# Optimization experiments

Measured on AMD Instinct MI355X. Metric: run time of the kernel, lower is better.

## Reference

```python
import jax, jax.numpy as jnp
import numpy as np

B, C, H = 4, 64, 48
HEADS, BSWIN = 2, 4
BIG = [3, 6, 12, 24]      # big window edge per scale (cubic)
SMALL = [1, 2, 4, 8]      # small (pool) window edge per scale
NH = 3                    # small windows per big window per dim (= big/small)
L = NH ** 3               # tokens per big window after pooling
CPH = C // (HEADS * BSWIN)  # channels per head per scale = 8


def _rel_pos_index():
    coords = np.stack(np.meshgrid(*([np.arange(NH)] * 3), indexing='ij')).reshape(3, -1)
    rel = coords[:, :, None] - coords[:, None, :] + (NH - 1)
    span = 2 * NH - 1
    return jnp.asarray(rel[0] * span * span + rel[1] * span + rel[2])  # (L, L) int

REL_IDX = _rel_pos_index()


def _interp_matrix(n_in, n_out):
    # 1D linear interpolation matrix, align_corners=True (matches F.interpolate)
    if n_out == n_in:
        return jnp.eye(n_in, dtype=jnp.float32)
    pos = jnp.arange(n_out, dtype=jnp.float32) * (n_in - 1) / (n_out - 1)
    i0 = jnp.clip(jnp.floor(pos).astype(jnp.int32), 0, n_in - 2)
    w = pos - i0.astype(jnp.float32)
    r = jnp.arange(n_out)
    m = jnp.zeros((n_out, n_in), jnp.float32)
    return m.at[r, i0].add(1.0 - w).at[r, i0 + 1].add(w)


def _gather(x):
    # x: (B, C, H, H, H) -> (B, HEADS, sum_N, L, CPH)
    b = x.shape[0]
    x = x.reshape(b, BSWIN, HEADS, CPH, H, H, H)
    parts, Ns = [], []
    for i in range(BSWIN):
        bw, sw = BIG[i], SMALL[i]
        N1 = H // bw
        xi = x[:, i].reshape(b, HEADS, CPH, N1, NH, sw, N1, NH, sw, N1, NH, sw)
        xi = xi.max(axis=(5, 8, 11))  # max-pool each small window
        # (b, head, c, Nh, nh, Nw, nw, Nd, nd) -> b head (Nh Nw Nd) (nh nw nd) c
        xi = xi.transpose(0, 1, 3, 5, 7, 4, 6, 8, 2)
        parts.append(xi.reshape(b, HEADS, N1 ** 3, L, CPH))
        Ns.append(N1)
    return jnp.concatenate(parts, axis=2), Ns


def _scatter(attn, Ns):
    # attn: (B, HEADS, sum_N, L, CPH) -> (B, C, H, H, H)
    b = attn.shape[0]
    outs, idx = [], 0
    for i in range(BSWIN):
        bw, sw = BIG[i], SMALL[i]
        N1 = Ns[i]
        N = N1 ** 3
        o = attn[:, :, idx:idx + N].reshape(b, HEADS, N, NH, NH, NH, CPH)
        M = _interp_matrix(NH, bw)  # trilinear upsample by small window size
        o = jnp.einsum('bhnijkc,pi,qj,rk->bhnpqrc', o, M, M, M)
        o = o.reshape(b, HEADS, N1, N1, N1, bw, bw, bw, CPH)
        # b head Nh Nw Nd wh ww wd c -> b head c (Nh wh) (Nw ww) (Nd wd)
        o = o.transpose(0, 1, 8, 2, 5, 3, 6, 4, 7).reshape(b, HEADS, CPH, H, H, H)
        outs.append(o)
        idx += N
    out = jnp.stack(outs, axis=1)  # b bswin head c h w d
    return out.reshape(b, C, H, H, H)


def _attention(q, k, v, rpb_table):
    c = q.shape[-1]
    scores = jnp.einsum('bhNmc,bhNnc->bhNmn', q, k) / jnp.sqrt(jnp.asarray(c, q.dtype))
    w = jax.nn.softmax(scores, axis=-1)
    bias = rpb_table[REL_IDX].transpose(2, 0, 1)  # (head, L, L), added POST-softmax
    w = w + bias[None, :, None]
    return jnp.einsum('bhNmn,bhNnc->bhNmc', w, v)


def setup_inputs() -> dict:
    key = jax.random.key(0)
    kq, kk, kv, kp = jax.random.split(key, 4)
    shp = (B, C, H, H, H)
    return {
        'query': jax.random.normal(kq, shp, jnp.float32),
        'key': jax.random.normal(kk, shp, jnp.float32),
        'value': jax.random.normal(kv, shp, jnp.float32),
        'rpb_table': jax.random.normal(kp, ((2 * NH - 1) ** 3, HEADS), jnp.float32) * 0.02,
    }


def reference(query, key, value, rpb_table):
    q, Ns = _gather(query)
    k, _ = _gather(key)
    v, _ = _gather(value)
    attn = _attention(q, k, v, rpb_table)
    return _scatter(attn, Ns)
```

## Files before the change

### kernel.cpp

```cpp
#include <hip/hip_runtime.h>


typedef unsigned short u16;
static constexpr long S1 = 4L * 48 * 24 * 24 * 24;

typedef float f4 __attribute__((ext_vector_type(4)));
typedef u16 us8 __attribute__((ext_vector_type(8)));
typedef u16 us4 __attribute__((ext_vector_type(4)));

__device__ __forceinline__ f4 ntload(const float* p) {
    return __builtin_nontemporal_load((const f4*)p);
}
__device__ __forceinline__ void ntstore(float* p, f4 v) {
    __builtin_nontemporal_store(v, (f4*)p);
}
__device__ __forceinline__ f4 vmax4(f4 a, f4 b) {
    f4 r;
    r[0] = fmaxf(a[0], b[0]); r[1] = fmaxf(a[1], b[1]);
    r[2] = fmaxf(a[2], b[2]); r[3] = fmaxf(a[3], b[3]);
    return r;
}
__device__ __forceinline__ float b2f(u16 u) {
    union { unsigned int i; float f; } c; c.i = ((unsigned int)u) << 16; return c.f;
}
__device__ __forceinline__ u16 f2b(float x) {
    union { float f; unsigned int i; } c; c.f = x;
    unsigned int b = c.i;
    return (u16)((b + 0x7FFFu + ((b >> 16) & 1u)) >> 16);
}

__device__ __forceinline__ void pool1_body(int pid,
                                           const float* __restrict__ q,
                                           const float* __restrict__ k,
                                           const float* __restrict__ v,
                                           u16* __restrict__ P1)
{
    const int tz = pid % 3;
    int rest = pid / 3;
    const int zc = rest % 12; rest /= 12;
    const int c = rest % 48;
    const int b = rest / 48;
    const float* in = tz == 0 ? q : (tz == 1 ? k : v);
    u16* o = P1 + (long)tz * S1;
    const float* base = in + ((long)b * 64 + 16 + c) * 110592;

    for (int i = threadIdx.x; i < 288; i += 256) {
        const int zl = i / 144;
        const int rem = i % 144;
        const int oy = rem / 6;
        const int qx = rem % 6;
        const int oz = zc * 2 + zl;
        const float* p = base + ((long)(2 * oz) * 48 + 2 * oy) * 48 + qx * 8;
        f4 r0a = ntload(p),        r0b = ntload(p + 4);
        f4 r1a = ntload(p + 48),   r1b = ntload(p + 52);
        f4 r2a = ntload(p + 2304), r2b = ntload(p + 2308);
        f4 r3a = ntload(p + 2352), r3b = ntload(p + 2356);
        f4 ma = vmax4(vmax4(r0a, r1a), vmax4(r2a, r3a));
        f4 mb = vmax4(vmax4(r0b, r1b), vmax4(r2b, r3b));
        us4 res;
        res[0] = f2b(fmaxf(ma[0], ma[1]));
        res[1] = f2b(fmaxf(ma[2], ma[3]));
        res[2] = f2b(fmaxf(mb[0], mb[1]));
        res[3] = f2b(fmaxf(mb[2], mb[3]));
        long oaddr = (((long)b * 48 + c) * 24 + oz) * 576 + oy * 24 + qx * 4;
        *(us4*)(o + oaddr) = res;
    }
}

__device__ __forceinline__ void attn0_body(int aid, float* smem,
                                           const float* __restrict__ qsrc,
                                           const float* __restrict__ ksrc,
                                           const float* __restrict__ vsrc,
                                           const float* __restrict__ rpb,
                                           float* __restrict__ out)
{
    float* tile = smem;
    float* bias = smem + 5376;
    const int tid = threadIdx.x;
    int rest = aid;
    const int half = rest & 1; rest >>= 1;
    const int Wy = rest % 16; rest /= 16;
    const int Wz = rest % 16; rest /= 16;
    const int head = rest % 2;
    const int b = rest / 2;

    for (int i = tid; i < 729; i += 256) {
        int m = i / 27, n = i % 27;
        int mi = m / 9, mj = (m / 3) % 3, mk = m % 3;
        int ni = n / 9, nj = (n / 3) % 3, nk = n % 3;
        int ridx = (mi - ni + 2) * 25 + (mj - nj + 2) * 5 + (mk - nk + 2);
        bias[i] = rpb[ridx * 2 + head];
    }

    for (int i = tid; i < 1296; i += 256) {
        int seg = i / 6;
        int off = (i % 6) * 4;
        int tz = seg / 72;
        int rem = seg % 72;
        int cph = rem / 9;
        int rem2 = rem % 9;
        int zt = rem2 / 3;
        int r = rem2 % 3;
        const float* src = tz == 0 ? qsrc : (tz == 1 ? ksrc : vsrc);
        long addr = ((((long)b * 64 + head * 8 + cph) * 48 + 3 * Wz + zt) * 48
                     + 3 * Wy + r) * 48 + half * 24 + off;
        f4 f = ntload(src + addr);
#pragma unroll
        for (int j = 0; j < 4; j++) {
            int xl = off + j;
            int wxl = xl / 3, tk = xl - wxl * 3;
            int tok = zt * 9 + r * 3 + tk;
            tile[((wxl * 3 + tz) * 8 + cph) * 28 + tok] = f[j];
        }
    }
    __syncthreads();

    const int wx = tid >> 5;
    const int lane = tid & 31;
    if (lane < 27) {
        const int m = lane;
        float* b0 = tile + wx * 672;
        const float* kb = b0 + 224;
        const float* vb = b0 + 448;
        float qr[8];
#pragma unroll
        for (int c = 0; c < 8; c++) qr[c] = b0[c * 28 + m];
        float s[27];
        float mx = -1e30f;
#pragma unroll
        for (int n = 0; n < 27; n++) {
            float acc = 0.f;
#pragma unroll
            for (int c = 0; c < 8; c++) acc += qr[c] * kb[c * 28 + n];
            acc *= 0.35355339059327373f;
            s[n] = acc;
            mx = fmaxf(mx, acc);
        }
        float sum = 0.f;
#pragma unroll
        for (int n = 0; n < 27; n++) {
            s[n] = __expf(s[n] - mx);
            sum += s[n];
        }
        float rs = 1.0f / sum;
        float o[8] = {0, 0, 0, 0, 0, 0, 0, 0};
#pragma unroll
        for (int n = 0; n < 27; n++) {
            float w = s[n] * rs + bias[m * 27 + n];
#pragma unroll
            for (int c = 0; c < 8; c++) o[c] += w * vb[c * 28 + n];
        }
#pragma unroll
        for (int c = 0; c < 8; c++) b0[c * 28 + m] = o[c];
    }
    __syncthreads();

    for (int i = tid; i < 432; i += 256) {
        int x4i = i % 6;
        int t2 = i / 6;
        int cph = t2 % 8; t2 /= 8;
        int y = t2 % 3;
        int zl = t2 / 3;
        f4 res;
#pragma unroll
        for (int e = 0; e < 4; e++) {
            int xl = x4i * 4 + e;
            int wxl = xl / 3, tk = xl - wxl * 3;
            int tok = zl * 9 + y * 3 + tk;
            res[e] = tile[wxl * 672 + cph * 28 + tok];
        }
        int z = 3 * Wz + zl;
        int Y = 3 * Wy + y;
        long oaddr = (((long)(b * 64 + head * 8 + cph) * 48 + z) * 48 + Y) * 48
                     + half * 24 + x4i * 4;
        ntstore(out + oaddr, res);
    }
}

__global__ void fused_k1(const float* __restrict__ q, const float* __restrict__ k,
                         const float* __restrict__ v, const float* __restrict__ rpb,
                         u16* __restrict__ P1, float* __restrict__ out)
{
    __shared__ __align__(16) float smem[6105];
    const int bx = blockIdx.x;
    if (bx < 8192 && (bx & 1) == 0) {
        attn0_body(bx >> 1, smem, q, k, v, rpb, out);
    } else {
        int pid = (bx < 8192) ? (bx >> 1) : (bx - 4096);
        pool1_body(pid, q, k, v, P1);
    }
}

static constexpr int WS = 676;

__device__ __forceinline__ void load_bias(float* bias, const float* __restrict__ rpb,
                                          int head, int tid)
{
    for (int i = tid; i < 729; i += 256) {
        int m = i / 27, n = i % 27;
        int mi = m / 9, mj = (m / 3) % 3, mk = m % 3;
        int ni = n / 9, nj = (n / 3) % 3, nk = n % 3;
        int ridx = (mi - ni + 2) * 25 + (mj - nj + 2) * 5 + (mk - nk + 2);
        bias[i] = rpb[ridx * 2 + head];
    }
}

__device__ __forceinline__ void attn_tile(float* tile, const float* bias, int tid, int NW)
{
    const int wx = tid >> 5;
    const int lane = tid & 31;
    if (wx < NW && lane < 27) {
        const int m = lane;
        float* b0 = tile + wx * WS;
        const float* kb = b0 + 224;
        const float* vb = b0 + 448;
        float qr[8];
#pragma unroll
        for (int c = 0; c < 8; c++) qr[c] = b0[c * 28 + m];
        float s[27];
        float mx = -1e30f;
#pragma unroll
        for (int n = 0; n < 27; n++) {
            float acc = 0.f;
#pragma unroll
            for (int c = 0; c < 8; c++) acc += qr[c] * kb[c * 28 + n];
            acc *= 0.35355339059327373f;
            s[n] = acc;
            mx = fmaxf(mx, acc);
        }
        float sum = 0.f;
#pragma unroll
        for (int n = 0; n < 27; n++) {
            s[n] = __expf(s[n] - mx);
            sum += s[n];
        }
        float rs = 1.0f / sum;
        float o[8] = {0, 0, 0, 0, 0, 0, 0, 0};
#pragma unroll
        for (int n = 0; n < 27; n++) {
            float w = s[n] * rs + bias[m * 27 + n];
#pragma unroll
            for (int c = 0; c < 8; c++) o[c] += w * vb[c * 28 + n];
        }
#pragma unroll
        for (int c = 0; c < 8; c++) b0[c * 28 + m] = o[c];
    }
}

__device__ __forceinline__ void preblend(const float* bp, int i0p, int i0q,
                                         float w00, float w01, float w10, float w11,
                                         float* v)
{
#pragma unroll
    for (int kx = 0; kx < 3; kx++) {
        const float* t = bp + i0p * 9 + i0q * 3 + kx;
        v[kx] = w00 * t[0] + w01 * t[3] + w10 * t[9] + w11 * t[12];
    }
}

__global__ void fused_k2(const u16* __restrict__ P1, const float* __restrict__ rpb,
                         float* __restrict__ out)
{
    __shared__ __align__(16) float smem[8 * WS + 729];
    float* tile = smem;
    float* bias = smem + 8 * WS;
    const int tid = threadIdx.x;
    const int bx = blockIdx.x;

    if (bx >= 1024) {
        int aid = bx - 1024;
        const int Wy = aid % 8; aid /= 8;
        const int Wz = aid % 8; aid /= 8;
        const int head = aid % 2;
        const int b = aid / 2;
        load_bias(bias, rpb, head, tid);
        for (int i = tid; i < 648; i += 256) {
            int xq = i % 3;
            int row = i / 3;
            int tz = row / 72;
            int rem = row % 72;
            int cph = rem / 9;
            int rem2 = rem % 9;
            int zt = rem2 / 3, r = rem2 % 3;
            const u16* p = P1 + (long)tz * S1 + ((long)b * 48 + head * 8 + cph) * 13824
                           + (3 * Wz + zt) * 576 + (3 * Wy + r) * 24 + xq * 8;
            us8 u = *(const us8*)p;
#pragma unroll
            for (int j = 0; j < 8; j++) {
                int xl = xq * 8 + j;
                int wxl = xl / 3, tk = xl - wxl * 3;
                tile[wxl * WS + (tz * 8 + cph) * 28 + zt * 9 + r * 3 + tk] = b2f(u[j]);
            }
        }
        __syncthreads();
        attn_tile(tile, bias, tid, 8);
        __syncthreads();

        const float inv = 2.0f / 5.0f;
        for (int i = tid; i < 3456; i += 256) {
            int x4 = i % 12;
            int t2 = i / 12;
            int cph = t2 % 8; t2 /= 8;
            int wq = t2 % 6;
            int wp = t2 / 6;
            float posp = wp * inv; int i0p = min((int)posp, 1); float fp = posp - (float)i0p;
            float posq = wq * inv; int i0q = min((int)posq, 1); float fq = posq - (float)i0q;
            float w00 = (1.f - fp) * (1.f - fq), w01 = (1.f - fp) * fq;
            float w10 = fp * (1.f - fq),         w11 = fp * fq;
            int Wa = (4 * x4) / 6, Wb = (4 * x4 + 3) / 6;
            float va[3], vb2[3];
            preblend(tile + Wa * WS + cph * 28, i0p, i0q, w00, w01, w10, w11, va);
            preblend(tile + Wb * WS + cph * 28, i0p, i0q, w00, w01, w10, w11, vb2);
            f4 res;
#pragma unroll
            for (int e = 0; e < 4; e++) {
                int xg = 4 * x4 + e;
                int Wx = xg / 6, wr = xg - 6 * Wx;
                const float* vv = (Wx == Wa) ? va : vb2;
                float posr = wr * inv; int i0r = min((int)posr, 1); float fr = posr - (float)i0r;
                res[e] = (1.f - fr) * vv[i0r] + fr * vv[i0r + 1];
            }
            long oaddr = (((long)(b * 64 + 16 + head * 8 + cph) * 48 + 6 * Wz + wp) * 48
                          + 6 * Wy + wq) * 48 + x4 * 4;
            ntstore(out + oaddr, res);
        }
    } else if (bx >= 512) {
        int bid = bx - 512;
        const int chunk = bid % 4; bid /= 4;
        const int Wy = bid % 4; bid /= 4;
        const int Wz = bid % 4; bid /= 4;
        const int head = bid % 2;
        const int b = bid / 2;
        load_bias(bias, rpb, head, tid);
        for (int i = tid; i < 648; i += 256) {
            int xq = i % 3;
            int t = i / 3;
            int yt = t % 3; t /= 3;
            int zt = t % 3; t /= 3;
            int cph = t % 8;
            int tz = t / 8;
            const u16* base = P1 + (long)tz * S1 + ((long)b * 48 + 16 + head * 8 + cph) * 13824;
            float tv[4] = {-1e30f, -1e30f, -1e30f, -1e30f};
#pragma unroll
            for (int dz = 0; dz < 2; dz++)
#pragma unroll
                for (int dy = 0; dy < 2; dy++) {
                    const u16* p = base + (6 * Wz + 2 * zt + dz) * 576
                                   + (6 * Wy + 2 * yt + dy) * 24 + xq * 8;
                    us8 u = *(const us8*)p;
#pragma unroll
                    for (int j = 0; j < 4; j++)
                        tv[j] = fmaxf(tv[j], fmaxf(b2f(u[2 * j]), b2f(u[2 * j + 1])));
                }
#pragma unroll
            for (int j = 0; j < 4; j++) {
                int xt = xq * 4 + j;
                int wxl = xt / 3, tk = xt - wxl * 3;
                tile[wxl * WS + (tz * 8 + cph) * 28 + zt * 9 + yt * 3 + tk] = tv[j];
            }
        }
        __syncthreads();
        attn_tile(tile, bias, tid, 4);
        __syncthreads();

        const float inv = 2.0f / 11.0f;
        for (int i = tid; i < 3456; i += 256) {
            int x4 = i % 12;
            int t2 = i / 12;
            int cph = t2 % 8; t2 /= 8;
            int wq = t2 % 12;
            int wp = chunk * 3 + t2 / 12;
            float posp = wp * inv; int i0p = min((int)posp, 1); float fp = posp - (float)i0p;
            float posq = wq * inv; int i0q = min((int)posq, 1); float fq = posq - (float)i0q;
            float w00 = (1.f - fp) * (1.f - fq), w01 = (1.f - fp) * fq;
            float w10 = fp * (1.f - fq),         w11 = fp * fq;
            int W = x4 / 3;
            float v[3];
            preblend(tile + W * WS + cph * 28, i0p, i0q, w00, w01, w10, w11, v);
            f4 res;
#pragma unroll
            for (int e = 0; e < 4; e++) {
                int xg = 4 * x4 + e;
                int wr = xg - 12 * W;
                float posr = wr * inv; int i0r = min((int)posr, 1); float fr = posr - (float)i0r;
                res[e] = (1.f - fr) * v[i0r] + fr * v[i0r + 1];
            }
            long oaddr = (((long)(b * 64 + 32 + head * 8 + cph) * 48 + 12 * Wz + wp) * 48
                          + 12 * Wy + wq) * 48 + x4 * 4;
            ntstore(out + oaddr, res);
        }
    } else {
        int cid = bx;
        const int slice = cid % 8; cid /= 8;
        const int Wx = cid % 2; cid /= 2;
        const int Wy = cid % 2; cid /= 2;
        const int Wz = cid % 2; cid /= 2;
        const int head = cid % 2;
        const int b = cid / 2;
        load_bias(bias, rpb, head, tid);
        for (int i = tid; i < 216; i += 256) {
            int yt = i % 3;
            int t = i / 3;
            int zt = t % 3; t /= 3;
            int cph = t % 8;
            int tz = t / 8;
            const u16* base = P1 + (long)tz * S1 + ((long)b * 48 + 32 + head * 8 + cph) * 13824;
            float tv[3] = {-1e30f, -1e30f, -1e30f};
#pragma unroll
            for (int dz = 0; dz < 4; dz++)
#pragma unroll
                for (int dy = 0; dy < 4; dy++) {
                    const u16* p = base + (12 * Wz + 4 * zt + dz) * 576
                                   + (12 * Wy + 4 * yt + dy) * 24 + 12 * Wx;
#pragma unroll
                    for (int s3 = 0; s3 < 3; s3++) {
                        us4 u = *(const us4*)(p + 4 * s3);
                        tv[s3] = fmaxf(tv[s3],
                                       fmaxf(fmaxf(b2f(u[0]), b2f(u[1])),
                                             fmaxf(b2f(u[2]), b2f(u[3]))));
                    }
                }
#pragma unroll
            for (int s3 = 0; s3 < 3; s3++)
                tile[(tz * 8 + cph) * 28 + zt * 9 + yt * 3 + s3] = tv[s3];
        }
        __syncthreads();
        attn_tile(tile, bias, tid, 1);
        __syncthreads();

        const float inv = 2.0f / 23.0f;
        for (int i = tid; i < 3456; i += 256) {
            int x4 = i % 6;
            int t2 = i / 6;
            int cph = t2 % 8; t2 /= 8;
            int wq = t2 % 24;
            int wp = slice * 3 + t2 / 24;
            float posp = wp * inv; int i0p = min((int)posp, 1); float fp = posp - (float)i0p;
            float posq = wq * inv; int i0q = min((int)posq, 1); float fq = posq - (float)i0q;
            float w00 = (1.f - fp) * (1.f - fq), w01 = (1.f - fp) * fq;
            float w10 = fp * (1.f - fq),         w11 = fp * fq;
            float v[3];
            preblend(tile + cph * 28, i0p, i0q, w00, w01, w10, w11, v);
            f4 res;
#pragma unroll
            for (int e = 0; e < 4; e++) {
                int wr = 4 * x4 + e;
                float posr = wr * inv; int i0r = min((int)posr, 1); float fr = posr - (float)i0r;
                res[e] = (1.f - fr) * v[i0r] + fr * v[i0r + 1];
            }
            long oaddr = (((long)(b * 64 + 48 + head * 8 + cph) * 48 + 24 * Wz + wp) * 48
                          + 24 * Wy + wq) * 48 + 24 * Wx + x4 * 4;
            ntstore(out + oaddr, res);
        }
    }
}

extern "C" void kernel_launch(void* const* d_in, const int* in_sizes, int n_in,
                              void* d_out, int out_size, void* d_ws, size_t ws_size,
                              hipStream_t stream)
{
    const float* q   = (const float*)d_in[0];
    const float* k   = (const float*)d_in[1];
    const float* v   = (const float*)d_in[2];
    const float* rpb = (const float*)d_in[3];
    float* out = (float*)d_out;
    u16* P1 = (u16*)d_ws;

    fused_k1<<<11008, 256, 0, stream>>>(q, k, v, rpb, P1, out);

    fused_k2<<<1536, 256, 0, stream>>>(P1, rpb, out);
}
```

Baseline: 161.6 us.

## Fuse both kernels into one launch, pooling directly from fp32 inputs

Replaces the two-kernel scheme with a single kernel. The old scheme pooled scales 1-3 into a bf16 workspace and then re-read it. Each scale's block now max-pools its own window straight from the fp32 q/k/v inputs, which removes the workspace round trip, the bf16 rounding and one launch. In exchange, the large-scale blocks become much heavier: 64 blocks each do a 24^3 window pool plus the full upsample, and 128 blocks do 4 windows each. This creates load imbalance and long tail blocks, though those heavy blocks are placed at the start of the grid.

Result: slower. 190.5 us (+17.9%).

```diff
diff --git a/kernel.cpp b/kernel.cpp
--- a/kernel.cpp
+++ b/kernel.cpp
@@ -1,12 +1,7 @@
 #include <hip/hip_runtime.h>
 
 
-typedef unsigned short u16;
-static constexpr long S1 = 4L * 48 * 24 * 24 * 24;
-
 typedef float f4 __attribute__((ext_vector_type(4)));
-typedef u16 us8 __attribute__((ext_vector_type(8)));
-typedef u16 us4 __attribute__((ext_vector_type(4)));
 
 __device__ __forceinline__ f4 ntload(const float* p) {
     return __builtin_nontemporal_load((const f4*)p);
@@ -20,50 +15,74 @@
     r[2] = fmaxf(a[2], b[2]); r[3] = fmaxf(a[3], b[3]);
     return r;
 }
-__device__ __forceinline__ float b2f(u16 u) {
-    union { unsigned int i; float f; } c; c.i = ((unsigned int)u) << 16; return c.f;
-}
-__device__ __forceinline__ u16 f2b(float x) {
-    union { float f; unsigned int i; } c; c.f = x;
-    unsigned int b = c.i;
-    return (u16)((b + 0x7FFFu + ((b >> 16) & 1u)) >> 16);
-}
-
-__device__ __forceinline__ void pool1_body(int pid,
-                                           const float* __restrict__ q,
-                                           const float* __restrict__ k,
-                                           const float* __restrict__ v,
-                                           u16* __restrict__ P1)
-{
-    const int tz = pid % 3;
-    int rest = pid / 3;
-    const int zc = rest % 12; rest /= 12;
-    const int c = rest % 48;
-    const int b = rest / 48;
-    const float* in = tz == 0 ? q : (tz == 1 ? k : v);
-    u16* o = P1 + (long)tz * S1;
-    const float* base = in + ((long)b * 64 + 16 + c) * 110592;
-
-    for (int i = threadIdx.x; i < 288; i += 256) {
-        const int zl = i / 144;
-        const int rem = i % 144;
-        const int oy = rem / 6;
-        const int qx = rem % 6;
-        const int oz = zc * 2 + zl;
-        const float* p = base + ((long)(2 * oz) * 48 + 2 * oy) * 48 + qx * 8;
-        f4 r0a = ntload(p),        r0b = ntload(p + 4);
-        f4 r1a = ntload(p + 48),   r1b = ntload(p + 52);
-        f4 r2a = ntload(p + 2304), r2b = ntload(p + 2308);
-        f4 r3a = ntload(p + 2352), r3b = ntload(p + 2356);
-        f4 ma = vmax4(vmax4(r0a, r1a), vmax4(r2a, r3a));
-        f4 mb = vmax4(vmax4(r0b, r1b), vmax4(r2b, r3b));
-        us4 res;
-        res[0] = f2b(fmaxf(ma[0], ma[1]));
-        res[1] = f2b(fmaxf(ma[2], ma[3]));
-        res[2] = f2b(fmaxf(mb[0], mb[1]));
-        res[3] = f2b(fmaxf(mb[2], mb[3]));
-        long oaddr = (((long)b * 48 + c) * 24 + oz) * 576 + oy * 24 + qx * 4;
-        *(us4*)(o + oaddr) = res;
+__device__ __forceinline__ float hmax4(f4 v) {
+    return fmaxf(fmaxf(v[0], v[1]), fmaxf(v[2], v[3]));
+}
+
+static constexpr int WS = 676;
+
+__device__ __forceinline__ void load_bias(float* bias, const float* __restrict__ rpb,
+                                          int head, int tid)
+{
+    for (int i = tid; i < 729; i += 256) {
+        int m = i / 27, n = i % 27;
+        int mi = m / 9, mj = (m / 3) % 3, mk = m % 3;
+        int ni = n / 9, nj = (n / 3) % 3, nk = n % 3;
+        int ridx = (mi - ni + 2) * 25 + (mj - nj + 2) * 5 + (mk - nk + 2);
+        bias[i] = rpb[ridx * 2 + head];
+    }
+}
+
+__device__ __forceinline__ void attn_tile(float* tile, const float* bias, int tid, int NW)
+{
+    const int wx = tid >> 5;
+    const int lane = tid & 31;
+    if (wx < NW && lane < 27) {
+        const int m = lane;
+        float* b0 = tile + wx * WS;
+        const float* kb = b0 + 224;
+        const float* vb = b0 + 448;
+        float qr[8];
+#pragma unroll
+        for (int c = 0; c < 8; c++) qr[c] = b0[c * 28 + m];
+        float s[27];
+        float mx = -1e30f;
+#pragma unroll
+        for (int n = 0; n < 27; n++) {
+            float acc = 0.f;
+#pragma unroll
+            for (int c = 0; c < 8; c++) acc += qr[c] * kb[c * 28 + n];
+            acc *= 0.35355339059327373f;
+            s[n] = acc;
+            mx = fmaxf(mx, acc);
+        }
+        float sum = 0.f;
+#pragma unroll
+        for (int n = 0; n < 27; n++) {
+            s[n] = __expf(s[n] - mx);
+            sum += s[n];
+        }
+        float rs = 1.0f / sum;
+        float o[8] = {0, 0, 0, 0, 0, 0, 0, 0};
+#pragma unroll
+        for (int n = 0; n < 27; n++) {
+            float w = s[n] * rs + bias[m * 27 + n];
+#pragma unroll
+            for (int c = 0; c < 8; c++) o[c] += w * vb[c * 28 + n];
+        }
+#pragma unroll
+        for (int c = 0; c < 8; c++) b0[c * 28 + m] = o[c];
+    }
+}
+
+__device__ __forceinline__ void preblend(const float* bp, int i0p, int i0q,
+                                         float w00, float w01, float w10, float w11,
+                                         float* v)
+{
+#pragma unroll
+    for (int kx = 0; kx < 3; kx++) {
+        const float* t = bp + i0p * 9 + i0q * 3 + kx;
+        v[kx] = w00 * t[0] + w01 * t[3] + w10 * t[9] + w11 * t[12];
     }
 }
 
@@ -177,119 +196,180 @@
     }
 }
 
-__global__ void fused_k1(const float* __restrict__ q, const float* __restrict__ k,
-                         const float* __restrict__ v, const float* __restrict__ rpb,
-                         u16* __restrict__ P1, float* __restrict__ out)
-{
-    __shared__ __align__(16) float smem[6105];
-    const int bx = blockIdx.x;
-    if (bx < 8192 && (bx & 1) == 0) {
-        attn0_body(bx >> 1, smem, q, k, v, rpb, out);
-    } else {
-        int pid = (bx < 8192) ? (bx >> 1) : (bx - 4096);
-        pool1_body(pid, q, k, v, P1);
-    }
-}
-
-static constexpr int WS = 676;
-
-__device__ __forceinline__ void load_bias(float* bias, const float* __restrict__ rpb,
-                                          int head, int tid)
-{
-    for (int i = tid; i < 729; i += 256) {
-        int m = i / 27, n = i % 27;
-        int mi = m / 9, mj = (m / 3) % 3, mk = m % 3;
-        int ni = n / 9, nj = (n / 3) % 3, nk = n % 3;
-        int ridx = (mi - ni + 2) * 25 + (mj - nj + 2) * 5 + (mk - nk + 2);
-        bias[i] = rpb[ridx * 2 + head];
-    }
-}
-
-__device__ __forceinline__ void attn_tile(float* tile, const float* bias, int tid, int NW)
-{
-    const int wx = tid >> 5;
-    const int lane = tid & 31;
-    if (wx < NW && lane < 27) {
-        const int m = lane;
-        float* b0 = tile + wx * WS;
-        const float* kb = b0 + 224;
-        const float* vb = b0 + 448;
-        float qr[8];
-#pragma unroll
-        for (int c = 0; c < 8; c++) qr[c] = b0[c * 28 + m];
-        float s[27];
-        float mx = -1e30f;
-#pragma unroll
-        for (int n = 0; n < 27; n++) {
-            float acc = 0.f;
-#pragma unroll
-            for (int c = 0; c < 8; c++) acc += qr[c] * kb[c * 28 + n];
-            acc *= 0.35355339059327373f;
-            s[n] = acc;
-            mx = fmaxf(mx, acc);
-        }
-        float sum = 0.f;
-#pragma unroll
-        for (int n = 0; n < 27; n++) {
-            s[n] = __expf(s[n] - mx);
-            sum += s[n];
-        }
-        float rs = 1.0f / sum;
-        float o[8] = {0, 0, 0, 0, 0, 0, 0, 0};
-#pragma unroll
-        for (int n = 0; n < 27; n++) {
-            float w = s[n] * rs + bias[m * 27 + n];
-#pragma unroll
-            for (int c = 0; c < 8; c++) o[c] += w * vb[c * 28 + n];
-        }
-#pragma unroll
-        for (int c = 0; c < 8; c++) b0[c * 28 + m] = o[c];
-    }
-}
-
-__device__ __forceinline__ void preblend(const float* bp, int i0p, int i0q,
-                                         float w00, float w01, float w10, float w11,
-                                         float* v)
-{
-#pragma unroll
-    for (int kx = 0; kx < 3; kx++) {
-        const float* t = bp + i0p * 9 + i0q * 3 + kx;
-        v[kx] = w00 * t[0] + w01 * t[3] + w10 * t[9] + w11 * t[12];
-    }
-}
-
-__global__ void fused_k2(const u16* __restrict__ P1, const float* __restrict__ rpb,
-                         float* __restrict__ out)
-{
-    __shared__ __align__(16) float smem[8 * WS + 729];
+__global__ void fused_all(const float* __restrict__ q, const float* __restrict__ k,
+                          const float* __restrict__ v, const float* __restrict__ rpb,
+                          float* __restrict__ out)
+{
+    __shared__ __align__(16) float smem[6137];
     float* tile = smem;
     float* bias = smem + 8 * WS;
     const int tid = threadIdx.x;
     const int bx = blockIdx.x;
 
-    if (bx >= 1024) {
-        int aid = bx - 1024;
+    if (bx >= 704) {
+        attn0_body(bx - 704, smem, q, k, v, rpb, out);
+        return;
+    }
+
+    if (bx < 64) {
+        int cid = bx;
+        const int Wx = cid % 2; cid /= 2;
+        const int Wy = cid % 2; cid /= 2;
+        const int Wz = cid % 2; cid /= 2;
+        const int head = cid % 2;
+        const int b = cid / 2;
+        load_bias(bias, rpb, head, tid);
+
+        for (int i = tid; i < 648; i += 256) {
+            int tok = i % 27;
+            int t = i / 27;
+            int cph = t % 8;
+            int tz = t / 8;
+            const int zt = tok / 9, yt = (tok / 3) % 3, xt = tok % 3;
+            const float* in = tz == 0 ? q : (tz == 1 ? k : v);
+            const float* base = in + (((long)b * 64 + 48 + head * 8 + cph) * 48
+                                      + Wz * 24 + zt * 8) * 2304
+                                + (long)(Wy * 24 + yt * 8) * 48 + Wx * 24 + xt * 8;
+            f4 acc = ntload(base);
+            acc = vmax4(acc, ntload(base + 4));
+            for (int dz = 0; dz < 8; dz++) {
+#pragma unroll
+                for (int dy = 0; dy < 8; dy++) {
+                    if (dz == 0 && dy == 0) continue;
+                    const float* p = base + dz * 2304 + dy * 48;
+                    acc = vmax4(acc, ntload(p));
+                    acc = vmax4(acc, ntload(p + 4));
+                }
+            }
+            tile[(tz * 8 + cph) * 28 + tok] = hmax4(acc);
+        }
+        __syncthreads();
+        attn_tile(tile, bias, tid, 1);
+        __syncthreads();
+
+        const float inv = 2.0f / 23.0f;
+        for (int i = tid; i < 27648; i += 256) {
+            int x4 = i % 6;
+            int t2 = i / 6;
+            int cph = t2 % 8; t2 /= 8;
+            int wq = t2 % 24;
+            int wp = t2 / 24;
+            float posp = wp * inv; int i0p = min((int)posp, 1); float fp = posp - (float)i0p;
+            float posq = wq * inv; int i0q = min((int)posq, 1); float fq = posq - (float)i0q;
+            float w00 = (1.f - fp) * (1.f - fq), w01 = (1.f - fp) * fq;
+            float w10 = fp * (1.f - fq),         w11 = fp * fq;
+            float vv[3];
+            preblend(tile + cph * 28, i0p, i0q, w00, w01, w10, w11, vv);
+            f4 res;
+#pragma unroll
+            for (int e = 0; e < 4; e++) {
+                int wr = 4 * x4 + e;
+                float posr = wr * inv; int i0r = min((int)posr, 1); float fr = posr - (float)i0r;
+                res[e] = (1.f - fr) * vv[i0r] + fr * vv[i0r + 1];
+            }
+            long oaddr = (((long)(b * 64 + 48 + head * 8 + cph) * 48 + 24 * Wz + wp) * 48
+                          + 24 * Wy + wq) * 48 + 24 * Wx + x4 * 4;
+            ntstore(out + oaddr, res);
+        }
+    } else if (bx < 192) {
+        int bid = bx - 64;
+        const int Wy = bid % 4; bid /= 4;
+        const int Wz = bid % 4; bid /= 4;
+        const int head = bid % 2;
+        const int b = bid / 2;
+        load_bias(bias, rpb, head, tid);
+
+        for (int i = tid; i < 1296; i += 256) {
+            int xp = i % 6;
+            int t = i / 6;
+            int yt = t % 3; t /= 3;
+            int zt = t % 3; t /= 3;
+            int cph = t % 8;
+            int tz = t / 8;
+            const float* in = tz == 0 ? q : (tz == 1 ? k : v);
+            const float* base = in + (((long)b * 64 + 32 + head * 8 + cph) * 48
+                                      + Wz * 12 + zt * 4) * 2304
+                                + (long)(Wy * 12 + yt * 4) * 48 + xp * 8;
+            f4 a0 = ntload(base), a1 = ntload(base + 4);
+#pragma unroll
+            for (int dz = 0; dz < 4; dz++) {
+#pragma unroll
+                for (int dy = 0; dy < 4; dy++) {
+                    if (dz == 0 && dy == 0) continue;
+                    const float* p = base + dz * 2304 + dy * 48;
+                    a0 = vmax4(a0, ntload(p));
+                    a1 = vmax4(a1, ntload(p + 4));
+                }
+            }
+            float tv[2] = {hmax4(a0), hmax4(a1)};
+#pragma unroll
+            for (int j = 0; j < 2; j++) {
+                int xl = xp * 2 + j;
+                int wxl = xl / 3, tk = xl - wxl * 3;
+                tile[wxl * WS + (tz * 8 + cph) * 28 + zt * 9 + yt * 3 + tk] = tv[j];
+            }
+        }
+        __syncthreads();
+        attn_tile(tile, bias, tid, 4);
+        __syncthreads();
+
+        const float inv = 2.0f / 11.0f;
+        for (int i = tid; i < 13824; i += 256) {
+            int x4 = i % 12;
+            int t2 = i / 12;
+            int cph = t2 % 8; t2 /= 8;
+            int wq = t2 % 12;
+            int wp = t2 / 12;
+            float posp = wp * inv; int i0p = min((int)posp, 1); float fp = posp - (float)i0p;
+            float posq = wq * inv; int i0q = min((int)posq, 1); float fq = posq - (float)i0q;
+            float w00 = (1.f - fp) * (1.f - fq), w01 = (1.f - fp) * fq;
+            float w10 = fp * (1.f - fq),         w11 = fp * fq;
+            int W = x4 / 3;
+            float vv[3];
+            preblend(tile + W * WS + cph * 28, i0p, i0q, w00, w01, w10, w11, vv);
+            f4 res;
+#pragma unroll
+            for (int e = 0; e < 4; e++) {
+                int wr = 4 * x4 + e - 12 * W;
+                float posr = wr * inv; int i0r = min((int)posr, 1); float fr = posr - (float)i0r;
+                res[e] = (1.f - fr) * vv[i0r] + fr * vv[i0r + 1];
+            }
+            long oaddr = (((long)(b * 64 + 32 + head * 8 + cph) * 48 + 12 * Wz + wp) * 48
+                          + 12 * Wy + wq) * 48 + x4 * 4;
+            ntstore(out + oaddr, res);
+        }
+    } else {
+        int aid = bx - 192;
         const int Wy = aid % 8; aid /= 8;
         const int Wz = aid % 8; aid /= 8;
         const int head = aid % 2;
         const int b = aid / 2;
         load_bias(bias, rpb, head, tid);
-        for (int i = tid; i < 648; i += 256) {
-            int xq = i % 3;
-            int row = i / 3;
-            int tz = row / 72;
-            int rem = row % 72;
-            int cph = rem / 9;
-            int rem2 = rem % 9;
-            int zt = rem2 / 3, r = rem2 % 3;
-            const u16* p = P1 + (long)tz * S1 + ((long)b * 48 + head * 8 + cph) * 13824
-                           + (3 * Wz + zt) * 576 + (3 * Wy + r) * 24 + xq * 8;
-            us8 u = *(const us8*)p;
-#pragma unroll
-            for (int j = 0; j < 8; j++) {
-                int xl = xq * 8 + j;
+
+        for (int i = tid; i < 1296; i += 256) {
+            int qx = i % 6;
+            int t = i / 6;
+            int yt = t % 3; t /= 3;
+            int zt = t % 3; t /= 3;
+            int cph = t % 8;
+            int tz = t / 8;
+            const float* in = tz == 0 ? q : (tz == 1 ? k : v);
+            const float* base = in + (((long)b * 64 + 16 + head * 8 + cph) * 48
+                                      + Wz * 6 + zt * 2) * 2304
+                                + (long)(Wy * 6 + yt * 2) * 48 + qx * 8;
+            f4 r0a = ntload(base),        r0b = ntload(base + 4);
+            f4 r1a = ntload(base + 48),   r1b = ntload(base + 52);
+            f4 r2a = ntload(base + 2304), r2b = ntload(base + 2308);
+            f4 r3a = ntload(base + 2352), r3b = ntload(base + 2356);
+            f4 ma = vmax4(vmax4(r0a, r1a), vmax4(r2a, r3a));
+            f4 mb = vmax4(vmax4(r0b, r1b), vmax4(r2b, r3b));
+            float tv[4] = { fmaxf(ma[0], ma[1]), fmaxf(ma[2], ma[3]),
+                            fmaxf(mb[0], mb[1]), fmaxf(mb[2], mb[3]) };
+#pragma unroll
+            for (int j = 0; j < 4; j++) {
+                int xl = qx * 4 + j;
                 int wxl = xl / 3, tk = xl - wxl * 3;
-                tile[wxl * WS + (tz * 8 + cph) * 28 + zt * 9 + r * 3 + tk] = b2f(u[j]);
+                tile[wxl * WS + (tz * 8 + cph) * 28 + zt * 9 + yt * 3 + tk] = tv[j];
             }
         }
         __syncthreads();
@@ -324,134 +404,6 @@
                           + 6 * Wy + wq) * 48 + x4 * 4;
             ntstore(out + oaddr, res);
         }
-    } else if (bx >= 512) {
-        int bid = bx - 512;
-        const int chunk = bid % 4; bid /= 4;
-        const int Wy = bid % 4; bid /= 4;
-        const int Wz = bid % 4; bid /= 4;
-        const int head = bid % 2;
-        const int b = bid / 2;
-        load_bias(bias, rpb, head, tid);
-        for (int i = tid; i < 648; i += 256) {
-            int xq = i % 3;
-            int t = i / 3;
-            int yt = t % 3; t /= 3;
-            int zt = t % 3; t /= 3;
-            int cph = t % 8;
-            int tz = t / 8;
-            const u16* base = P1 + (long)tz * S1 + ((long)b * 48 + 16 + head * 8 + cph) * 13824;
-            float tv[4] = {-1e30f, -1e30f, -1e30f, -1e30f};
-#pragma unroll
-            for (int dz = 0; dz < 2; dz++)
-#pragma unroll
-                for (int dy = 0; dy < 2; dy++) {
-                    const u16* p = base + (6 * Wz + 2 * zt + dz) * 576
-                                   + (6 * Wy + 2 * yt + dy) * 24 + xq * 8;
-                    us8 u = *(const us8*)p;
-#pragma unroll
-                    for (int j = 0; j < 4; j++)
-                        tv[j] = fmaxf(tv[j], fmaxf(b2f(u[2 * j]), b2f(u[2 * j + 1])));
-                }
-#pragma unroll
-            for (int j = 0; j < 4; j++) {
-                int xt = xq * 4 + j;
-                int wxl = xt / 3, tk = xt - wxl * 3;
-                tile[wxl * WS + (tz * 8 + cph) * 28 + zt * 9 + yt * 3 + tk] = tv[j];
-            }
-        }
-        __syncthreads();
-        attn_tile(tile, bias, tid, 4);
-        __syncthreads();
-
-        const float inv = 2.0f / 11.0f;
-        for (int i = tid; i < 3456; i += 256) {
-            int x4 = i % 12;
-            int t2 = i / 12;
-            int cph = t2 % 8; t2 /= 8;
-            int wq = t2 % 12;
-            int wp = chunk * 3 + t2 / 12;
-            float posp = wp * inv; int i0p = min((int)posp, 1); float fp = posp - (float)i0p;
-            float posq = wq * inv; int i0q = min((int)posq, 1); float fq = posq - (float)i0q;
-            float w00 = (1.f - fp) * (1.f - fq), w01 = (1.f - fp) * fq;
-            float w10 = fp * (1.f - fq),         w11 = fp * fq;
-            int W = x4 / 3;
-            float v[3];
-            preblend(tile + W * WS + cph * 28, i0p, i0q, w00, w01, w10, w11, v);
-            f4 res;
-#pragma unroll
-            for (int e = 0; e < 4; e++) {
-                int xg = 4 * x4 + e;
-                int wr = xg - 12 * W;
-                float posr = wr * inv; int i0r = min((int)posr, 1); float fr = posr - (float)i0r;
-                res[e] = (1.f - fr) * v[i0r] + fr * v[i0r + 1];
-            }
-            long oaddr = (((long)(b * 64 + 32 + head * 8 + cph) * 48 + 12 * Wz + wp) * 48
-                          + 12 * Wy + wq) * 48 + x4 * 4;
-            ntstore(out + oaddr, res);
-        }
-    } else {
-        int cid = bx;
-        const int slice = cid % 8; cid /= 8;
-        const int Wx = cid % 2; cid /= 2;
-        const int Wy = cid % 2; cid /= 2;
-        const int Wz = cid % 2; cid /= 2;
-        const int head = cid % 2;
-        const int b = cid / 2;
-        load_bias(bias, rpb, head, tid);
-        for (int i = tid; i < 216; i += 256) {
-            int yt = i % 3;
-            int t = i / 3;
-            int zt = t % 3; t /= 3;
-            int cph = t % 8;
-            int tz = t / 8;
-            const u16* base = P1 + (long)tz * S1 + ((long)b * 48 + 32 + head * 8 + cph) * 13824;
-            float tv[3] = {-1e30f, -1e30f, -1e30f};
-#pragma unroll
-            for (int dz = 0; dz < 4; dz++)
-#pragma unroll
-                for (int dy = 0; dy < 4; dy++) {
-                    const u16* p = base + (12 * Wz + 4 * zt + dz) * 576
-                                   + (12 * Wy + 4 * yt + dy) * 24 + 12 * Wx;
-#pragma unroll
-                    for (int s3 = 0; s3 < 3; s3++) {
-                        us4 u = *(const us4*)(p + 4 * s3);
-                        tv[s3] = fmaxf(tv[s3],
-                                       fmaxf(fmaxf(b2f(u[0]), b2f(u[1])),
-                                             fmaxf(b2f(u[2]), b2f(u[3]))));
-                    }
-                }
-#pragma unroll
-            for (int s3 = 0; s3 < 3; s3++)
-                tile[(tz * 8 + cph) * 28 + zt * 9 + yt * 3 + s3] = tv[s3];
-        }
-        __syncthreads();
-        attn_tile(tile, bias, tid, 1);
-        __syncthreads();
-
-        const float inv = 2.0f / 23.0f;
-        for (int i = tid; i < 3456; i += 256) {
-            int x4 = i % 6;
-            int t2 = i / 6;
-            int cph = t2 % 8; t2 /= 8;
-            int wq = t2 % 24;
-            int wp = slice * 3 + t2 / 24;
-            float posp = wp * inv; int i0p = min((int)posp, 1); float fp = posp - (float)i0p;
-            float posq = wq * inv; int i0q = min((int)posq, 1); float fq = posq - (float)i0q;
-            float w00 = (1.f - fp) * (1.f - fq), w01 = (1.f - fp) * fq;
-            float w10 = fp * (1.f - fq),         w11 = fp * fq;
-            float v[3];
-            preblend(tile + cph * 28, i0p, i0q, w00, w01, w10, w11, v);
-            f4 res;
-#pragma unroll
-            for (int e = 0; e < 4; e++) {
-                int wr = 4 * x4 + e;
-                float posr = wr * inv; int i0r = min((int)posr, 1); float fr = posr - (float)i0r;
-                res[e] = (1.f - fr) * v[i0r] + fr * v[i0r + 1];
-            }
-            long oaddr = (((long)(b * 64 + 48 + head * 8 + cph) * 48 + 24 * Wz + wp) * 48
-                          + 24 * Wy + wq) * 48 + 24 * Wx + x4 * 4;
-            ntstore(out + oaddr, res);
-        }
     }
 }
 
@@ -464,9 +416,6 @@
     const float* v   = (const float*)d_in[2];
     const float* rpb = (const float*)d_in[3];
     float* out = (float*)d_out;
-    u16* P1 = (u16*)d_ws;
-
-    fused_k1<<<11008, 256, 0, stream>>>(q, k, v, rpb, P1, out);
-
-    fused_k2<<<1536, 256, 0, stream>>>(P1, rpb, out);
-}
+
+    fused_all<<<4800, 256, 0, stream>>>(q, k, v, rpb, out);
+}
```
